# Performance work log

Measured on AMD Instinct MI355X. Metric: run time of the kernel, lower is better.

Reference implementation:

```python
import jax, jax.numpy as jnp
import numpy as np

N = 50000      # nodes
E = 800000     # edges
F = 128        # num_features
H = 128        # hidden_channels
L = 3          # num_layers
P = 32         # num_partitions
EPS = 1e-5     # BatchNorm1d eps


def _batchnorm(h):
    # BatchNorm1d(affine=False, track_running_stats=False): batch stats, biased var
    m = jnp.mean(h, axis=0)
    v = jnp.var(h, axis=0)
    return (h - m) * jax.lax.rsqrt(v + EPS)


def setup_inputs() -> dict:
    key = jax.random.key(0)
    ks = jax.random.split(key, 12)
    x = jax.random.normal(ks[0], (N, F), dtype=jnp.float32)
    edge_index = jax.random.randint(ks[1], (2, E), 0, N)
    edge_weights = jax.random.uniform(ks[2], (E,), dtype=jnp.float32)
    partitions = (jax.random.uniform(ks[3], (N, P)) < (1.0 / P)).astype(jnp.float32)
    node_weights = jax.random.uniform(ks[4], (N,), dtype=jnp.float32)
    edge_curr_node = jax.random.uniform(ks[5], (N,), dtype=jnp.float32)
    conv_w = 0.05 * jax.random.normal(ks[6], (L, F, H), dtype=jnp.float32)
    conv_b = jnp.zeros((L, H), dtype=jnp.float32)
    lin1_w = 0.05 * jax.random.normal(ks[7], (4 * H, H), dtype=jnp.float32)
    lin1_b = jnp.zeros((H,), dtype=jnp.float32)
    lin2_w = 0.05 * jax.random.normal(ks[8], (H, 1), dtype=jnp.float32)
    lin2_b = jnp.zeros((1,), dtype=jnp.float32)
    return {"x": x, "edge_index": edge_index, "edge_weights": edge_weights,
            "partitions": partitions, "node_weights": node_weights,
            "edge_curr_node": edge_curr_node, "conv_w": conv_w, "conv_b": conv_b,
            "lin1_w": lin1_w, "lin1_b": lin1_b, "lin2_w": lin2_w,
            "lin2_b": lin2_b, "curr_node_id": 123}


def reference(x, edge_index, edge_weights, partitions, node_weights,
              edge_curr_node, conv_w, conv_b, lin1_w, lin1_b, lin2_w, lin2_b,
              curr_node_id):
    src, dst = edge_index[0], edge_index[1]
    # GCN normalization with added self-loops (weight 1)
    deg = jax.ops.segment_sum(edge_weights, dst, num_segments=N) + 1.0
    dinv = jax.lax.rsqrt(deg)
    norm = dinv[src] * edge_weights * dinv[dst]          # [E]
    self_norm = (dinv * dinv)[:, None]                   # [N,1]

    h = x
    for l in range(L):
        hw = h @ conv_w[l] + conv_b[l]                   # [N,H]
        agg = jax.ops.segment_sum(hw[src] * norm[:, None], dst, num_segments=N)
        agg = agg + hw * self_norm                       # self-loop term
        h = jax.nn.relu(_batchnorm(agg))

    x_curr = h[curr_node_id]                             # [H]
    # mlp scoring: concat [h | x_curr | edge_col repeated to 2H] -> [N,4H]
    cat = jnp.concatenate([
        h,
        jnp.broadcast_to(x_curr[None, :], (N, H)),
        jnp.broadcast_to(edge_curr_node[:, None], (N, 2 * H)),
    ], axis=1)
    scores = jax.nn.relu(cat @ lin1_w + lin1_b) @ lin2_w + lin2_b  # [N,1]
    # pool == 'sum'
    partition_scores = scores.T @ partitions             # [1,P]
    return (partition_scores, h)
```

## Files before the change

### kernel.cpp

```cpp
#include <hip/hip_runtime.h>

#define N_NODES 50000
#define N_EDGES 800000
#define NP 50048
#define MAXDEG 64
#define PADK 136
#define NCOPY 64
#define WPB 512
#define NBUK 196
#define BCAP 6144
#define EBB 782

typedef __bf16 bf16_8 __attribute__((ext_vector_type(8)));
typedef float  f32_4  __attribute__((ext_vector_type(4)));

__device__ inline float2 bf2f2(unsigned int u) {
    union { unsigned int i; float f; } a, b;
    a.i = u << 16;
    b.i = u & 0xffff0000u;
    return make_float2(a.f, b.f);
}

__global__ void k_init_wprep(float* __restrict__ colpart, float* __restrict__ out_head,
                             const float* __restrict__ conv_w, const float* __restrict__ lin1_w,
                             __bf16* __restrict__ WT, float* __restrict__ svec,
                             int* __restrict__ bcnt) {
    int b = blockIdx.x, t = threadIdx.x;
    if (b < WPB) {
        int mat = b >> 7, n = b & 127;
        if (t < 128) {
            const float* srcm = (mat < 3) ? (conv_w + (size_t)mat * 16384) : lin1_w;
            WT[((size_t)mat * 128 + n) * 128 + t] = (__bf16)srcm[(size_t)t * 128 + n];
        }
    } else if (b == WPB) {
        if (t < 128) {
            float s = 0.f;
            for (int k = 256; k < 512; ++k) s += lin1_w[(size_t)k * 128 + t];
            svec[t] = s;
        }
    } else if (b < WPB + 65) {
        int i = (b - WPB - 1) * 256 + t;
        colpart[i] = 0.f;
    } else {
        if (t < 32) out_head[t] = 0.f;
        for (int i = t; i < NBUK * 16; i += 256) bcnt[i] = 0;
    }
}

__global__ __launch_bounds__(1024) void k_bucket(const int* __restrict__ src,
                                                 const int* __restrict__ dst,
                                                 const float* __restrict__ ew,
                                                 int* __restrict__ bcnt,
                                                 uint2* __restrict__ ebuf) {
    __shared__ uint2 stage[1024];
    __shared__ int cnt[NBUK], cnt2[NBUK], lstart[NBUK], gb[NBUK];
    __shared__ int wtot[4];
    int t = threadIdx.x;
    int e0 = blockIdx.x * 1024;
    int tot = min(1024, N_EDGES - e0);
    if (t < NBUK) { cnt[t] = 0; cnt2[t] = 0; }
    __syncthreads();
    uint2 rec = make_uint2(0u, 0u); int b = -1;
    if (t < tot) {
        int e = e0 + t;
        unsigned s = (unsigned)src[e], d = (unsigned)dst[e];
        rec = make_uint2(s | (d << 16), __float_as_uint(ew[e]));
        b = (int)(d >> 8);
        atomicAdd(&cnt[b], 1);
    }
    __syncthreads();
    int c = (t < NBUK) ? cnt[t] : 0;
    int x = c;
#pragma unroll
    for (int d2 = 1; d2 < 64; d2 <<= 1) {
        int v = __shfl_up(x, d2, 64);
        if ((t & 63) >= d2) x += v;
    }
    if ((t & 63) == 63 && t < 256) wtot[t >> 6] = x;
    if (t < NBUK && c > 0) gb[t] = atomicAdd(&bcnt[t * 16], c);
    __syncthreads();
    if (t < NBUK) {
        int pre = x - c;
        for (int w = 0; w < (t >> 6); ++w) pre += wtot[w];
        lstart[t] = pre;
    }
    __syncthreads();
    if (t < tot) {
        int r = atomicAdd(&cnt2[b], 1);
        stage[lstart[b] + r] = rec;
    }
    __syncthreads();
    if (t < tot) {
        uint2 v = stage[t];
        int bb = (int)(v.x >> 24);
        int idx = gb[bb] + (t - lstart[bb]);
        if (idx < BCAP) ebuf[(size_t)bb * BCAP + idx] = v;
    }
}

__global__ __launch_bounds__(256) void k_build(const int* __restrict__ bcnt,
                                               const uint2* __restrict__ ebuf,
                                               uint2* __restrict__ esn,
                                               int* __restrict__ fillp,
                                               float* __restrict__ dinv) {
    __shared__ int cnt[256];
    __shared__ float wsum[256];
    int t = threadIdx.x, b = blockIdx.x;
    cnt[t] = 0; wsum[t] = 0.f;
    __syncthreads();
    int m = min(bcnt[b * 16], BCAP);
    for (int i = t; i < m; i += 256) {
        uint2 rec = ebuf[(size_t)b * BCAP + i];
        int d = (int)(rec.x >> 16);
        int local = d & 255;
        int pos = atomicAdd(&cnt[local], 1);
        if (pos < MAXDEG)
            esn[(size_t)d * MAXDEG + pos] = make_uint2(rec.x & 0xffffu, rec.y);
        atomicAdd(&wsum[local], __uint_as_float(rec.y));
    }
    __syncthreads();
    int gn = b * 256 + t;
    if (gn < N_NODES) {
        fillp[gn] = cnt[t];
        dinv[gn] = rsqrtf(1.0f + wsum[t]);
    }
}

__global__ __launch_bounds__(256) void k_wnorm(uint2* __restrict__ esn,
                                               const int* __restrict__ fillp,
                                               const float* __restrict__ dinv) {
    int t = threadIdx.x;
    int n = (blockIdx.x * 256 + t) >> 6;
    int lane = t & 63;
    if (n >= N_NODES) return;
    int num = min(fillp[n], MAXDEG);
    if (lane < num) {
        uint2 e = esn[(size_t)n * MAXDEG + lane];
        float w = dinv[(int)e.x] * __uint_as_float(e.y) * dinv[n];
        esn[(size_t)n * MAXDEG + lane] = make_uint2(e.x, __float_as_uint(w));
    }
}

template <int AMODE>
__global__ __launch_bounds__(256) void k_gemm_mfma(const float* __restrict__ A,
                                                   const float* __restrict__ mean,
                                                   const float* __restrict__ rstd,
                                                   const __bf16* __restrict__ WT,
                                                   const float* __restrict__ bias,
                                                   __bf16* __restrict__ C, int nrows) {
    __shared__ __bf16 As[64 * PADK];
    __shared__ __bf16 Ws[128 * PADK];
    int t = threadIdx.x;
    int rowBase = blockIdx.x * 64;
    const uint4* WTg = (const uint4*)WT;
    for (int i = t; i < 2048; i += 256) {
        int n = i >> 4, k8 = i & 15;
        *(uint4*)&Ws[n * PADK + k8 * 8] = WTg[i];
    }
    const float4* A4 = (const float4*)A;
    const float4* M4 = (const float4*)mean;
    const float4* R4 = (const float4*)rstd;
    for (int i = t; i < 1024; i += 256) {
        int r = i >> 4, k8 = i & 15;
        int gr = rowBase + r;
        float4 a0 = make_float4(0.f, 0.f, 0.f, 0.f), a1 = a0;
        if (gr < nrows) {
            a0 = A4[(size_t)gr * 32 + k8 * 2];
            a1 = A4[(size_t)gr * 32 + k8 * 2 + 1];
        }
        if (AMODE == 1) {
            float4 m0 = M4[k8 * 2], m1 = M4[k8 * 2 + 1];
            float4 r0 = R4[k8 * 2], r1 = R4[k8 * 2 + 1];
            a0.x = fmaxf((a0.x - m0.x) * r0.x, 0.f); a0.y = fmaxf((a0.y - m0.y) * r0.y, 0.f);
            a0.z = fmaxf((a0.z - m0.z) * r0.z, 0.f); a0.w = fmaxf((a0.w - m0.w) * r0.w, 0.f);
            a1.x = fmaxf((a1.x - m1.x) * r1.x, 0.f); a1.y = fmaxf((a1.y - m1.y) * r1.y, 0.f);
            a1.z = fmaxf((a1.z - m1.z) * r1.z, 0.f); a1.w = fmaxf((a1.w - m1.w) * r1.w, 0.f);
        }
        bf16_8 o = { (__bf16)a0.x, (__bf16)a0.y, (__bf16)a0.z, (__bf16)a0.w,
                     (__bf16)a1.x, (__bf16)a1.y, (__bf16)a1.z, (__bf16)a1.w };
        *(bf16_8*)&As[r * PADK + k8 * 8] = o;
    }
    __syncthreads();
    int wave = t >> 6, lane = t & 63, quad = lane >> 4, m = lane & 15;
    int ar = wave * 16 + m;
    f32_4 acc[8];
#pragma unroll
    for (int i = 0; i < 8; ++i) acc[i] = (f32_4){0.f, 0.f, 0.f, 0.f};
#pragma unroll
    for (int kk = 0; kk < 4; ++kk) {
        bf16_8 a = *(const bf16_8*)&As[ar * PADK + kk * 32 + quad * 8];
#pragma unroll
        for (int n0 = 0; n0 < 8; ++n0) {
            bf16_8 b = *(const bf16_8*)&Ws[(n0 * 16 + m) * PADK + kk * 32 + quad * 8];
            acc[n0] = __builtin_amdgcn_mfma_f32_16x16x32_bf16(a, b, acc[n0], 0, 0, 0);
        }
    }
    __syncthreads();
#pragma unroll
    for (int n0 = 0; n0 < 8; ++n0) {
        int col = n0 * 16 + m;
        float bi = bias[col];
#pragma unroll
        for (int r = 0; r < 4; ++r) {
            int rr = wave * 16 + quad * 4 + r;
            As[rr * PADK + col] = (__bf16)(acc[n0][r] + bi);
        }
    }
    __syncthreads();
    uint4* Cg = (uint4*)C;
    for (int i = t; i < 1024; i += 256) {
        int r = i >> 4, k8 = i & 15;
        int gr = rowBase + r;
        if (gr < nrows) Cg[(size_t)gr * 16 + k8] = *(const uint4*)&As[r * PADK + k8 * 8];
    }
}

__global__ __launch_bounds__(256) void k_agg(const __bf16* __restrict__ hwb,
                                             const uint2* __restrict__ esn,
                                             const int* __restrict__ fillp,
                                             const float* __restrict__ dinv,
                                             float* __restrict__ agg,
                                             float* __restrict__ colpart) {
    __shared__ float red1[4 * 128], red2[4 * 128];
    int t = threadIdx.x;
    int n = (blockIdx.x * 256 + t) >> 6;
    int lane = t & 63, wave = t >> 6;
    float2 acc = make_float2(0.f, 0.f);
    const unsigned int* hw32 = (const unsigned int*)hwb;
    if (n < N_NODES) {
        float dvn = dinv[n];
        float2 sv = bf2f2(hw32[(size_t)n * 64 + lane]);
        acc.x = sv.x * dvn * dvn; acc.y = sv.y * dvn * dvn;
        int num = min(fillp[n], MAXDEG);
        int s_l = 0; float w_l = 0.f;
        if (lane < num) {
            uint2 e = esn[(size_t)n * MAXDEG + lane];
            s_l = (int)e.x;
            w_l = __uint_as_float(e.y);
        }
        int i = 0;
        for (; i + 8 <= num; i += 8) {
            int ss[8]; float ww[8]; unsigned uu[8];
#pragma unroll
            for (int j = 0; j < 8; ++j) { ss[j] = __shfl(s_l, i + j); ww[j] = __shfl(w_l, i + j); }
#pragma unroll
            for (int j = 0; j < 8; ++j) uu[j] = hw32[(size_t)ss[j] * 64 + lane];
#pragma unroll
            for (int j = 0; j < 8; ++j) {
                float2 f = bf2f2(uu[j]);
                acc.x += f.x * ww[j]; acc.y += f.y * ww[j];
            }
        }
        for (; i < num; ++i) {
            int s = __shfl(s_l, i);
            float w = __shfl(w_l, i);
            float2 f = bf2f2(hw32[(size_t)s * 64 + lane]);
            acc.x += f.x * w; acc.y += f.y * w;
        }
        ((float2*)agg)[(size_t)n * 64 + lane] = acc;
    }
    *(float2*)&red1[wave * 128 + 2 * lane] = acc;
    *(float2*)&red2[wave * 128 + 2 * lane] = make_float2(acc.x * acc.x, acc.y * acc.y);
    __syncthreads();
    if (t < 128) {
        float s = red1[t] + red1[128 + t] + red1[256 + t] + red1[384 + t];
        float q = red2[t] + red2[128 + t] + red2[256 + t] + red2[384 + t];
        int c = blockIdx.x & (NCOPY - 1);
        unsafeAtomicAdd(&colpart[c * 128 + t], s);
        unsafeAtomicAdd(&colpart[NCOPY * 128 + c * 128 + t], q);
    }
}

__global__ void k_bnfinal(float* colpart, float* mean, float* rstd) {
    int j = threadIdx.x;
    float s = 0.f, q = 0.f;
    for (int c = 0; c < NCOPY; ++c) {
        s += colpart[c * 128 + j];
        q += colpart[NCOPY * 128 + c * 128 + j];
        colpart[c * 128 + j] = 0.f;
        colpart[NCOPY * 128 + c * 128 + j] = 0.f;
    }
    float m = s * (1.0f / N_NODES);
    float v = q * (1.0f / N_NODES) - m * m;
    mean[j] = m;
    rstd[j] = rsqrtf(v + 1e-5f);
}

__global__ void k_prep(const float* __restrict__ agg, const float* __restrict__ mean,
                       const float* __restrict__ rstd, const int* __restrict__ cid,
                       const float* __restrict__ lin1w, const float* __restrict__ lin1b,
                       float* c0) {
    __shared__ float xc[128];
    int t = threadIdx.x;
    int cn = cid[0];
    float a = agg[(size_t)cn * 128 + t];
    xc[t] = fmaxf((a - mean[t]) * rstd[t], 0.f);
    __syncthreads();
    float acc = lin1b[t];
    for (int k = 0; k < 128; ++k)
        acc += xc[k] * lin1w[(size_t)(128 + k) * 128 + t];
    c0[t] = acc;
}

__global__ __launch_bounds__(256) void k_score_mfma(const float* __restrict__ agg,
                                                    const float* __restrict__ mean,
                                                    const float* __restrict__ rstd,
                                                    const __bf16* __restrict__ WT,
                                                    const float* __restrict__ c0,
                                                    const float* __restrict__ svec,
                                                    const float* __restrict__ ecn,
                                                    const float* __restrict__ lin2w,
                                                    const float* __restrict__ lin2b,
                                                    float* __restrict__ scores,
                                                    float* __restrict__ hout,
                                                    int nrows) {
    __shared__ __bf16 As[64 * PADK];
    __shared__ __bf16 Ws[128 * PADK];
    __shared__ float c0s[128], svs[128], l2s[128];
    int t = threadIdx.x;
    int rowBase = blockIdx.x * 64;
    const uint4* WTg = (const uint4*)WT;
    for (int i = t; i < 2048; i += 256) {
        int n = i >> 4, k8 = i & 15;
        *(uint4*)&Ws[n * PADK + k8 * 8] = WTg[i];
    }
    const float4* A4 = (const float4*)agg;
    const float4* M4 = (const float4*)mean;
    const float4* R4 = (const float4*)rstd;
    float4* H4 = (float4*)hout;
    for (int i = t; i < 1024; i += 256) {
        int r = i >> 4, k8 = i & 15;
        int gr = rowBase + r;
        float4 a0 = make_float4(0.f, 0.f, 0.f, 0.f), a1 = a0;
        if (gr < nrows) {
            a0 = A4[(size_t)gr * 32 + k8 * 2];
            a1 = A4[(size_t)gr * 32 + k8 * 2 + 1];
        }
        float4 m0 = M4[k8 * 2], m1 = M4[k8 * 2 + 1];
        float4 r0 = R4[k8 * 2], r1 = R4[k8 * 2 + 1];
        float4 f0, f1;
        f0.x = fmaxf((a0.x - m0.x) * r0.x, 0.f); f0.y = fmaxf((a0.y - m0.y) * r0.y, 0.f);
        f0.z = fmaxf((a0.z - m0.z) * r0.z, 0.f); f0.w = fmaxf((a0.w - m0.w) * r0.w, 0.f);
        f1.x = fmaxf((a1.x - m1.x) * r1.x, 0.f); f1.y = fmaxf((a1.y - m1.y) * r1.y, 0.f);
        f1.z = fmaxf((a1.z - m1.z) * r1.z, 0.f); f1.w = fmaxf((a1.w - m1.w) * r1.w, 0.f);
        if (gr < nrows) {
            H4[(size_t)gr * 32 + k8 * 2] = f0;
            H4[(size_t)gr * 32 + k8 * 2 + 1] = f1;
        }
        bf16_8 o = { (__bf16)f0.x, (__bf16)f0.y, (__bf16)f0.z, (__bf16)f0.w,
                     (__bf16)f1.x, (__bf16)f1.y, (__bf16)f1.z, (__bf16)f1.w };
        *(bf16_8*)&As[r * PADK + k8 * 8] = o;
    }
    if (t < 128) { c0s[t] = c0[t]; svs[t] = svec[t]; l2s[t] = lin2w[t]; }
    __syncthreads();
    int wave = t >> 6, lane = t & 63, quad = lane >> 4, m = lane & 15;
    int ar = wave * 16 + m;
    f32_4 acc[8];
#pragma unroll
    for (int i = 0; i < 8; ++i) acc[i] = (f32_4){0.f, 0.f, 0.f, 0.f};
#pragma unroll
    for (int kk = 0; kk < 4; ++kk) {
        bf16_8 a = *(const bf16_8*)&As[ar * PADK + kk * 32 + quad * 8];
#pragma unroll
        for (int n0 = 0; n0 < 8; ++n0) {
            bf16_8 b = *(const bf16_8*)&Ws[(n0 * 16 + m) * PADK + kk * 32 + quad * 8];
            acc[n0] = __builtin_amdgcn_mfma_f32_16x16x32_bf16(a, b, acc[n0], 0, 0, 0);
        }
    }
    float l2b = lin2b[0];
#pragma unroll
    for (int r = 0; r < 4; ++r) {
        int row = rowBase + wave * 16 + quad * 4 + r;
        float e = (row < nrows) ? ecn[row] : 0.f;
        float partial = 0.f;
#pragma unroll
        for (int n0 = 0; n0 < 8; ++n0) {
            int col = n0 * 16 + m;
            float v = acc[n0][r] + c0s[col] + e * svs[col];
            partial += fmaxf(v, 0.f) * l2s[col];
        }
        partial += __shfl_xor(partial, 8, 16);
        partial += __shfl_xor(partial, 4, 16);
        partial += __shfl_xor(partial, 2, 16);
        partial += __shfl_xor(partial, 1, 16);
        if (m == 0 && row < nrows) scores[row] = partial + l2b;
    }
}

__global__ void k_partition(const float* __restrict__ scores, const float* __restrict__ part,
                            float* out) {
    __shared__ float red[256];
    int t = threadIdx.x;
    int p = t & 31, rg = t >> 5;
    float acc = 0.f;
    for (int r = blockIdx.x * 8 + rg; r < N_NODES; r += gridDim.x * 8)
        acc += scores[r] * part[(size_t)r * 32 + p];
    red[t] = acc;
    __syncthreads();
    if (t < 32) {
        float s = 0.f;
        for (int i = 0; i < 8; ++i) s += red[i * 32 + t];
        unsafeAtomicAdd(&out[t], s);
    }
}

extern "C" void kernel_launch(void* const* d_in, const int* in_sizes, int n_in,
                              void* d_out, int out_size, void* d_ws, size_t ws_size,
                              hipStream_t stream) {
    const float* x        = (const float*)d_in[0];
    const int*   eidx     = (const int*)d_in[1];
    const float* ew       = (const float*)d_in[2];
    const float* parts    = (const float*)d_in[3];
    const float* ecn      = (const float*)d_in[5];
    const float* conv_w   = (const float*)d_in[6];
    const float* conv_b   = (const float*)d_in[7];
    const float* lin1_w   = (const float*)d_in[8];
    const float* lin1_b   = (const float*)d_in[9];
    const float* lin2_w   = (const float*)d_in[10];
    const float* lin2_b   = (const float*)d_in[11];
    const int*   cid      = (const int*)d_in[12];

    const int* src = eidx;
    const int* dst = eidx + N_EDGES;

    char* p = (char*)d_ws;
    auto alloc = [&](size_t bytes) { char* r = p; p += (bytes + 255) & ~size_t(255); return r; };
    int*    fillp   = (int*)alloc((size_t)NP * 4);
    uint2*  esn     = (uint2*)alloc((size_t)N_NODES * MAXDEG * 8);
    float*  dinv    = (float*)alloc(NP * 4);
    float*  scores  = (float*)alloc(NP * 4);
    float*  colpart = (float*)alloc(2 * NCOPY * 128 * 4);
    float*  mean    = (float*)alloc(128 * 4);
    float*  rstd    = (float*)alloc(128 * 4);
    float*  c0      = (float*)alloc(128 * 4);
    float*  svec    = (float*)alloc(128 * 4);
    __bf16* WT      = (__bf16*)alloc(4 * 128 * 128 * 2);
    __bf16* hwb     = (__bf16*)alloc((size_t)N_NODES * 128 * 2);
    float*  agg     = (float*)alloc((size_t)N_NODES * 128 * 4);
    int*    bcnt    = (int*)alloc((size_t)NBUK * 16 * 4);
    uint2*  ebuf    = (uint2*)alloc((size_t)NBUK * BCAP * 8);

    float* out_head = (float*)d_out;
    float* hbuf     = (float*)d_out + 32;

    const int GB = (N_NODES + 63) / 64;
    const int AB = (N_NODES * 64 + 255) / 256;

    k_init_wprep<<<WPB + 66, 256, 0, stream>>>(colpart, out_head, conv_w, lin1_w, WT, svec, bcnt);
    k_bucket<<<EBB, 1024, 0, stream>>>(src, dst, ew, bcnt, ebuf);
    k_build<<<NBUK, 256, 0, stream>>>(bcnt, ebuf, esn, fillp, dinv);
    k_wnorm<<<AB, 256, 0, stream>>>(esn, fillp, dinv);

    for (int l = 0; l < 3; ++l) {
        if (l == 0)
            k_gemm_mfma<0><<<GB, 256, 0, stream>>>(x, mean, rstd, WT, conv_b, hwb, N_NODES);
        else
            k_gemm_mfma<1><<<GB, 256, 0, stream>>>(agg, mean, rstd, WT + (size_t)l * 16384,
                                                   conv_b + (size_t)l * 128, hwb, N_NODES);
        k_agg<<<AB, 256, 0, stream>>>(hwb, esn, fillp, dinv, agg, colpart);
        k_bnfinal<<<1, 128, 0, stream>>>(colpart, mean, rstd);
    }

    k_prep<<<1, 128, 0, stream>>>(agg, mean, rstd, cid, lin1_w, lin1_b, c0);
    k_score_mfma<<<GB, 256, 0, stream>>>(agg, mean, rstd, WT + (size_t)3 * 16384, c0, svec,
                                         ecn, lin2_w, lin2_b, scores, hbuf, N_NODES);
    k_partition<<<256, 256, 0, stream>>>(scores, parts, out_head);
}
```

Measured before the change: 347.8 us.

## Gather 16-byte neighbor rows in aggregation and fuse edge-normalization into first GEMM

The aggregation kernel now gives each lane 8 bf16 features loaded as a uint4, so each wave processes 4 neighbors at once in 16-lane groups. The partial sums are then combined with cross-lane xor shuffles, which cuts the number of gather instructions and shuffles per edge. Separately, the edge-weight normalization kernel becomes extra blocks appended to the layer-0 GEMM launch, which removes one launch and lets that work overlap with the GEMM. The cost is more registers per thread, the shuffle reduction overhead, and shared-memory declarations in the normalization blocks that they do not use.

```diff
diff --git a/kernel.cpp b/kernel.cpp
--- a/kernel.cpp
+++ b/kernel.cpp
@@ -126,31 +126,32 @@
     }
 }
 
-__global__ __launch_bounds__(256) void k_wnorm(uint2* __restrict__ esn,
-                                               const int* __restrict__ fillp,
-                                               const float* __restrict__ dinv) {
-    int t = threadIdx.x;
-    int n = (blockIdx.x * 256 + t) >> 6;
-    int lane = t & 63;
-    if (n >= N_NODES) return;
-    int num = min(fillp[n], MAXDEG);
-    if (lane < num) {
-        uint2 e = esn[(size_t)n * MAXDEG + lane];
-        float w = dinv[(int)e.x] * __uint_as_float(e.y) * dinv[n];
-        esn[(size_t)n * MAXDEG + lane] = make_uint2(e.x, __float_as_uint(w));
-    }
-}
-
 template <int AMODE>
 __global__ __launch_bounds__(256) void k_gemm_mfma(const float* __restrict__ A,
                                                    const float* __restrict__ mean,
                                                    const float* __restrict__ rstd,
                                                    const __bf16* __restrict__ WT,
                                                    const float* __restrict__ bias,
-                                                   __bf16* __restrict__ C, int nrows) {
+                                                   __bf16* __restrict__ C, int nrows,
+                                                   uint2* __restrict__ esn,
+                                                   const int* __restrict__ fillp,
+                                                   const float* __restrict__ dinv,
+                                                   int gemmBlocks) {
     __shared__ __bf16 As[64 * PADK];
     __shared__ __bf16 Ws[128 * PADK];
     int t = threadIdx.x;
+    if (AMODE == 0 && blockIdx.x >= gemmBlocks) {
+        int n = ((blockIdx.x - gemmBlocks) * 256 + t) >> 6;
+        int lane = t & 63;
+        if (n >= N_NODES) return;
+        int num = min(fillp[n], MAXDEG);
+        if (lane < num) {
+            uint2 e = esn[(size_t)n * MAXDEG + lane];
+            float w = dinv[(int)e.x] * __uint_as_float(e.y) * dinv[n];
+            esn[(size_t)n * MAXDEG + lane] = make_uint2(e.x, __float_as_uint(w));
+        }
+        return;
+    }
     int rowBase = blockIdx.x * 64;
     const uint4* WTg = (const uint4*)WT;
     for (int i = t; i < 2048; i += 256) {
@@ -225,42 +226,80 @@
     int t = threadIdx.x;
     int n = (blockIdx.x * 256 + t) >> 6;
     int lane = t & 63, wave = t >> 6;
-    float2 acc = make_float2(0.f, 0.f);
-    const unsigned int* hw32 = (const unsigned int*)hwb;
+    int rs = lane >> 4, c16 = lane & 15;
+    float acc[8];
+#pragma unroll
+    for (int k = 0; k < 8; ++k) acc[k] = 0.f;
+    const uint4* hwq = (const uint4*)hwb;
     if (n < N_NODES) {
+        int num = min(fillp[n], MAXDEG);
         float dvn = dinv[n];
-        float2 sv = bf2f2(hw32[(size_t)n * 64 + lane]);
-        acc.x = sv.x * dvn * dvn; acc.y = sv.y * dvn * dvn;
-        int num = min(fillp[n], MAXDEG);
+        uint4 sv = hwq[(size_t)n * 16 + c16];
         int s_l = 0; float w_l = 0.f;
         if (lane < num) {
             uint2 e = esn[(size_t)n * MAXDEG + lane];
             s_l = (int)e.x;
             w_l = __uint_as_float(e.y);
         }
-        int i = 0;
-        for (; i + 8 <= num; i += 8) {
-            int ss[8]; float ww[8]; unsigned uu[8];
-#pragma unroll
-            for (int j = 0; j < 8; ++j) { ss[j] = __shfl(s_l, i + j); ww[j] = __shfl(w_l, i + j); }
-#pragma unroll
-            for (int j = 0; j < 8; ++j) uu[j] = hw32[(size_t)ss[j] * 64 + lane];
-#pragma unroll
-            for (int j = 0; j < 8; ++j) {
-                float2 f = bf2f2(uu[j]);
-                acc.x += f.x * ww[j]; acc.y += f.y * ww[j];
+        int groups = (num + 3) >> 2;
+        int g = 0;
+        for (; g + 4 <= groups; g += 4) {
+            uint4 u[4]; float w[4];
+#pragma unroll
+            for (int j = 0; j < 4; ++j) {
+                int idx = (g + j) * 4 + rs;
+                int s = __shfl(s_l, idx, 64);
+                w[j] = __shfl(w_l, idx, 64);
+                u[j] = hwq[(size_t)s * 16 + c16];
             }
-        }
-        for (; i < num; ++i) {
-            int s = __shfl(s_l, i);
-            float w = __shfl(w_l, i);
-            float2 f = bf2f2(hw32[(size_t)s * 64 + lane]);
-            acc.x += f.x * w; acc.y += f.y * w;
-        }
-        ((float2*)agg)[(size_t)n * 64 + lane] = acc;
-    }
-    *(float2*)&red1[wave * 128 + 2 * lane] = acc;
-    *(float2*)&red2[wave * 128 + 2 * lane] = make_float2(acc.x * acc.x, acc.y * acc.y);
+#pragma unroll
+            for (int j = 0; j < 4; ++j) {
+                float2 f0 = bf2f2(u[j].x), f1 = bf2f2(u[j].y);
+                float2 f2 = bf2f2(u[j].z), f3 = bf2f2(u[j].w);
+                acc[0] += f0.x * w[j]; acc[1] += f0.y * w[j];
+                acc[2] += f1.x * w[j]; acc[3] += f1.y * w[j];
+                acc[4] += f2.x * w[j]; acc[5] += f2.y * w[j];
+                acc[6] += f3.x * w[j]; acc[7] += f3.y * w[j];
+            }
+        }
+        for (; g < groups; ++g) {
+            int idx = g * 4 + rs;
+            int s = __shfl(s_l, idx, 64);
+            float w = __shfl(w_l, idx, 64);
+            uint4 u = hwq[(size_t)s * 16 + c16];
+            float2 f0 = bf2f2(u.x), f1 = bf2f2(u.y), f2 = bf2f2(u.z), f3 = bf2f2(u.w);
+            acc[0] += f0.x * w; acc[1] += f0.y * w;
+            acc[2] += f1.x * w; acc[3] += f1.y * w;
+            acc[4] += f2.x * w; acc[5] += f2.y * w;
+            acc[6] += f3.x * w; acc[7] += f3.y * w;
+        }
+#pragma unroll
+        for (int k = 0; k < 8; ++k) {
+            acc[k] += __shfl_xor(acc[k], 16, 64);
+            acc[k] += __shfl_xor(acc[k], 32, 64);
+        }
+        float d2 = dvn * dvn;
+        float2 s0 = bf2f2(sv.x), s1 = bf2f2(sv.y), s2 = bf2f2(sv.z), s3 = bf2f2(sv.w);
+        acc[0] += s0.x * d2; acc[1] += s0.y * d2;
+        acc[2] += s1.x * d2; acc[3] += s1.y * d2;
+        acc[4] += s2.x * d2; acc[5] += s2.y * d2;
+        acc[6] += s3.x * d2; acc[7] += s3.y * d2;
+        if (rs < 2) {
+            float4 o = make_float4(acc[rs * 4 + 0], acc[rs * 4 + 1],
+                                   acc[rs * 4 + 2], acc[rs * 4 + 3]);
+            ((float4*)agg)[(size_t)n * 32 + c16 * 2 + rs] = o;
+        }
+    }
+    if (rs == 0) {
+        *(float4*)&red1[wave * 128 + c16 * 8 + 0] =
+            make_float4(acc[0], acc[1], acc[2], acc[3]);
+        *(float4*)&red1[wave * 128 + c16 * 8 + 4] =
+            make_float4(acc[4], acc[5], acc[6], acc[7]);
+        *(float4*)&red2[wave * 128 + c16 * 8 + 0] =
+            make_float4(acc[0] * acc[0], acc[1] * acc[1], acc[2] * acc[2], acc[3] * acc[3]);
+        *(float4*)&red2[wave * 128 + c16 * 8 + 4] =
+            make_float4(acc[4] * acc[4], acc[5] * acc[5], acc[6] * acc[6], acc[7] * acc[7]);
+    }
     __syncthreads();
     if (t < 128) {
         float s = red1[t] + red1[128 + t] + red1[256 + t] + red1[384 + t];
@@ -449,14 +488,15 @@
     k_init_wprep<<<WPB + 66, 256, 0, stream>>>(colpart, out_head, conv_w, lin1_w, WT, svec, bcnt);
     k_bucket<<<EBB, 1024, 0, stream>>>(src, dst, ew, bcnt, ebuf);
     k_build<<<NBUK, 256, 0, stream>>>(bcnt, ebuf, esn, fillp, dinv);
-    k_wnorm<<<AB, 256, 0, stream>>>(esn, fillp, dinv);
 
     for (int l = 0; l < 3; ++l) {
         if (l == 0)
-            k_gemm_mfma<0><<<GB, 256, 0, stream>>>(x, mean, rstd, WT, conv_b, hwb, N_NODES);
+            k_gemm_mfma<0><<<GB + AB, 256, 0, stream>>>(x, mean, rstd, WT, conv_b, hwb, N_NODES,
+                                                        esn, fillp, dinv, GB);
         else
             k_gemm_mfma<1><<<GB, 256, 0, stream>>>(agg, mean, rstd, WT + (size_t)l * 16384,
-                                                   conv_b + (size_t)l * 128, hwb, N_NODES);
+                                                   conv_b + (size_t)l * 128, hwb, N_NODES,
+                                                   nullptr, nullptr, nullptr, GB);
         k_agg<<<AB, 256, 0, stream>>>(hwb, esn, fillp, dinv, agg, colpart);
         k_bnfinal<<<1, 128, 0, stream>>>(colpart, mean, rstd);
     }
```

New measurement: 344.3 us. Within noise of the previous version (-1.0%).

## Pack edges into CSR layout, fuse weight-normalization into first GEMM, split aggregation by feature chunk

Applied to the files above, without the earlier changes.

Replaces the padded per-node 64-slot edge array with a compact CSR-style packed array built by a prefix scan in k_build. The separate edge-weight normalization kernel is folded into extra blocks of the first GEMM launch, which removes one launch and lets that work overlap the GEMM. k_agg is restructured so each block handles one 32-column feature chunk, with blocks mapped across XCDs by chunk for better L2 locality of the gathered rows. Each wave processes four edges at a time in 16-lane groups and combines them with cross-lane shuffles. This adds launch blocks and shuffle reductions in exchange for less padded memory traffic and better cache reuse.

```diff
diff --git a/kernel.cpp b/kernel.cpp
--- a/kernel.cpp
+++ b/kernel.cpp
@@ -10,6 +10,7 @@
 #define NBUK 196
 #define BCAP 6144
 #define EBB 782
+#define AGB 50000
 
 typedef __bf16 bf16_8 __attribute__((ext_vector_type(8)));
 typedef float  f32_4  __attribute__((ext_vector_type(4)));
@@ -100,44 +101,50 @@
 
 __global__ __launch_bounds__(256) void k_build(const int* __restrict__ bcnt,
                                                const uint2* __restrict__ ebuf,
-                                               uint2* __restrict__ esn,
+                                               uint2* __restrict__ packed,
+                                               int* __restrict__ rowofs,
                                                int* __restrict__ fillp,
                                                float* __restrict__ dinv) {
     __shared__ int cnt[256];
     __shared__ float wsum[256];
+    __shared__ int pos[256];
+    __shared__ int wtot[4];
     int t = threadIdx.x, b = blockIdx.x;
     cnt[t] = 0; wsum[t] = 0.f;
     __syncthreads();
     int m = min(bcnt[b * 16], BCAP);
     for (int i = t; i < m; i += 256) {
         uint2 rec = ebuf[(size_t)b * BCAP + i];
-        int d = (int)(rec.x >> 16);
-        int local = d & 255;
-        int pos = atomicAdd(&cnt[local], 1);
-        if (pos < MAXDEG)
-            esn[(size_t)d * MAXDEG + pos] = make_uint2(rec.x & 0xffffu, rec.y);
+        int local = (int)(rec.x >> 16) & 255;
+        atomicAdd(&cnt[local], 1);
         atomicAdd(&wsum[local], __uint_as_float(rec.y));
     }
     __syncthreads();
+    int c = cnt[t];
+    int x = c;
+#pragma unroll
+    for (int d2 = 1; d2 < 64; d2 <<= 1) {
+        int v = __shfl_up(x, d2, 64);
+        if ((t & 63) >= d2) x += v;
+    }
+    if ((t & 63) == 63) wtot[t >> 6] = x;
+    __syncthreads();
+    int pre = x - c;
+    for (int w = 0; w < (t >> 6); ++w) pre += wtot[w];
+    int rstart = b * BCAP + pre;
+    pos[t] = rstart;
+    __syncthreads();
+    for (int i = t; i < m; i += 256) {
+        uint2 rec = ebuf[(size_t)b * BCAP + i];
+        int local = (int)(rec.x >> 16) & 255;
+        int p = atomicAdd(&pos[local], 1);
+        packed[p] = make_uint2(rec.x & 0xffffu, rec.y);
+    }
     int gn = b * 256 + t;
     if (gn < N_NODES) {
-        fillp[gn] = cnt[t];
+        fillp[gn] = c;
+        rowofs[gn] = rstart;
         dinv[gn] = rsqrtf(1.0f + wsum[t]);
-    }
-}
-
-__global__ __launch_bounds__(256) void k_wnorm(uint2* __restrict__ esn,
-                                               const int* __restrict__ fillp,
-                                               const float* __restrict__ dinv) {
-    int t = threadIdx.x;
-    int n = (blockIdx.x * 256 + t) >> 6;
-    int lane = t & 63;
-    if (n >= N_NODES) return;
-    int num = min(fillp[n], MAXDEG);
-    if (lane < num) {
-        uint2 e = esn[(size_t)n * MAXDEG + lane];
-        float w = dinv[(int)e.x] * __uint_as_float(e.y) * dinv[n];
-        esn[(size_t)n * MAXDEG + lane] = make_uint2(e.x, __float_as_uint(w));
     }
 }
 
@@ -147,10 +154,28 @@
                                                    const float* __restrict__ rstd,
                                                    const __bf16* __restrict__ WT,
                                                    const float* __restrict__ bias,
-                                                   __bf16* __restrict__ C, int nrows) {
+                                                   __bf16* __restrict__ C, int nrows,
+                                                   uint2* __restrict__ packed,
+                                                   const int* __restrict__ rowofs,
+                                                   const int* __restrict__ fillp,
+                                                   const float* __restrict__ dinv,
+                                                   int gemmBlocks) {
     __shared__ __bf16 As[64 * PADK];
     __shared__ __bf16 Ws[128 * PADK];
     int t = threadIdx.x;
+    if (AMODE == 0 && blockIdx.x >= gemmBlocks) {
+        int n = ((blockIdx.x - gemmBlocks) * 256 + t) >> 6;
+        int lane = t & 63;
+        if (n >= N_NODES) return;
+        int num = min(fillp[n], MAXDEG);
+        if (lane < num) {
+            int ro = rowofs[n];
+            uint2 e = packed[ro + lane];
+            float w = dinv[(int)e.x] * __uint_as_float(e.y) * dinv[n];
+            packed[ro + lane] = make_uint2(e.x, __float_as_uint(w));
+        }
+        return;
+    }
     int rowBase = blockIdx.x * 64;
     const uint4* WTg = (const uint4*)WT;
     for (int i = t; i < 2048; i += 256) {
@@ -216,58 +241,79 @@
 }
 
 __global__ __launch_bounds__(256) void k_agg(const __bf16* __restrict__ hwb,
-                                             const uint2* __restrict__ esn,
+                                             const uint2* __restrict__ packed,
+                                             const int* __restrict__ rowofs,
                                              const int* __restrict__ fillp,
                                              const float* __restrict__ dinv,
                                              float* __restrict__ agg,
                                              float* __restrict__ colpart) {
-    __shared__ float red1[4 * 128], red2[4 * 128];
+    __shared__ float red1[4 * 32], red2[4 * 32];
     int t = threadIdx.x;
-    int n = (blockIdx.x * 256 + t) >> 6;
+    int bi = blockIdx.x;
+    int xcd = bi & 7;
+    int chunk = xcd >> 1;
+    int nb = (bi >> 3) * 2 + (xcd & 1);
     int lane = t & 63, wave = t >> 6;
+    int e4 = lane >> 4, f16 = lane & 15;
+    int n = nb * 4 + wave;
     float2 acc = make_float2(0.f, 0.f);
     const unsigned int* hw32 = (const unsigned int*)hwb;
-    if (n < N_NODES) {
+    {
+        int num = min(fillp[n], MAXDEG);
+        int ro = rowofs[n];
         float dvn = dinv[n];
-        float2 sv = bf2f2(hw32[(size_t)n * 64 + lane]);
-        acc.x = sv.x * dvn * dvn; acc.y = sv.y * dvn * dvn;
-        int num = min(fillp[n], MAXDEG);
+        unsigned sv = hw32[(size_t)n * 64 + chunk * 16 + f16];
         int s_l = 0; float w_l = 0.f;
         if (lane < num) {
-            uint2 e = esn[(size_t)n * MAXDEG + lane];
+            uint2 e = packed[ro + lane];
             s_l = (int)e.x;
             w_l = __uint_as_float(e.y);
         }
-        int i = 0;
-        for (; i + 8 <= num; i += 8) {
-            int ss[8]; float ww[8]; unsigned uu[8];
-#pragma unroll
-            for (int j = 0; j < 8; ++j) { ss[j] = __shfl(s_l, i + j); ww[j] = __shfl(w_l, i + j); }
-#pragma unroll
-            for (int j = 0; j < 8; ++j) uu[j] = hw32[(size_t)ss[j] * 64 + lane];
-#pragma unroll
-            for (int j = 0; j < 8; ++j) {
-                float2 f = bf2f2(uu[j]);
-                acc.x += f.x * ww[j]; acc.y += f.y * ww[j];
+        int groups = (num + 3) >> 2;
+        int g = 0;
+        for (; g + 4 <= groups; g += 4) {
+            unsigned u[4]; float w[4];
+#pragma unroll
+            for (int j = 0; j < 4; ++j) {
+                int idx = (g + j) * 4 + e4;
+                int s = __shfl(s_l, idx, 64);
+                w[j] = __shfl(w_l, idx, 64);
+                u[j] = hw32[(size_t)s * 64 + chunk * 16 + f16];
             }
-        }
-        for (; i < num; ++i) {
-            int s = __shfl(s_l, i);
-            float w = __shfl(w_l, i);
-            float2 f = bf2f2(hw32[(size_t)s * 64 + lane]);
+#pragma unroll
+            for (int j = 0; j < 4; ++j) {
+                float2 f = bf2f2(u[j]);
+                acc.x += f.x * w[j]; acc.y += f.y * w[j];
+            }
+        }
+        for (; g < groups; ++g) {
+            int idx = g * 4 + e4;
+            int s = __shfl(s_l, idx, 64);
+            float w = __shfl(w_l, idx, 64);
+            float2 f = bf2f2(hw32[(size_t)s * 64 + chunk * 16 + f16]);
             acc.x += f.x * w; acc.y += f.y * w;
         }
-        ((float2*)agg)[(size_t)n * 64 + lane] = acc;
-    }
-    *(float2*)&red1[wave * 128 + 2 * lane] = acc;
-    *(float2*)&red2[wave * 128 + 2 * lane] = make_float2(acc.x * acc.x, acc.y * acc.y);
-    __syncthreads();
-    if (t < 128) {
-        float s = red1[t] + red1[128 + t] + red1[256 + t] + red1[384 + t];
-        float q = red2[t] + red2[128 + t] + red2[256 + t] + red2[384 + t];
+        acc.x += __shfl_xor(acc.x, 16, 64); acc.y += __shfl_xor(acc.y, 16, 64);
+        acc.x += __shfl_xor(acc.x, 32, 64); acc.y += __shfl_xor(acc.y, 32, 64);
+        float d2 = dvn * dvn;
+        float2 s0 = bf2f2(sv);
+        acc.x += s0.x * d2; acc.y += s0.y * d2;
+        if (e4 == 0)
+            ((float2*)agg)[(size_t)n * 64 + chunk * 16 + f16] = acc;
+    }
+    if (e4 == 0) {
+        red1[wave * 32 + f16 * 2]     = acc.x;
+        red1[wave * 32 + f16 * 2 + 1] = acc.y;
+        red2[wave * 32 + f16 * 2]     = acc.x * acc.x;
+        red2[wave * 32 + f16 * 2 + 1] = acc.y * acc.y;
+    }
+    __syncthreads();
+    if (t < 32) {
+        float s = red1[t] + red1[32 + t] + red1[64 + t] + red1[96 + t];
+        float q = red2[t] + red2[32 + t] + red2[64 + t] + red2[96 + t];
         int c = blockIdx.x & (NCOPY - 1);
-        unsafeAtomicAdd(&colpart[c * 128 + t], s);
-        unsafeAtomicAdd(&colpart[NCOPY * 128 + c * 128 + t], q);
+        unsafeAtomicAdd(&colpart[c * 128 + chunk * 32 + t], s);
+        unsafeAtomicAdd(&colpart[NCOPY * 128 + c * 128 + chunk * 32 + t], q);
     }
 }
 
@@ -426,7 +472,8 @@
     char* p = (char*)d_ws;
     auto alloc = [&](size_t bytes) { char* r = p; p += (bytes + 255) & ~size_t(255); return r; };
     int*    fillp   = (int*)alloc((size_t)NP * 4);
-    uint2*  esn     = (uint2*)alloc((size_t)N_NODES * MAXDEG * 8);
+    int*    rowofs  = (int*)alloc((size_t)NP * 4);
+    uint2*  packed  = (uint2*)alloc((size_t)NBUK * BCAP * 8);
     float*  dinv    = (float*)alloc(NP * 4);
     float*  scores  = (float*)alloc(NP * 4);
     float*  colpart = (float*)alloc(2 * NCOPY * 128 * 4);
@@ -448,16 +495,17 @@
 
     k_init_wprep<<<WPB + 66, 256, 0, stream>>>(colpart, out_head, conv_w, lin1_w, WT, svec, bcnt);
     k_bucket<<<EBB, 1024, 0, stream>>>(src, dst, ew, bcnt, ebuf);
-    k_build<<<NBUK, 256, 0, stream>>>(bcnt, ebuf, esn, fillp, dinv);
-    k_wnorm<<<AB, 256, 0, stream>>>(esn, fillp, dinv);
+    k_build<<<NBUK, 256, 0, stream>>>(bcnt, ebuf, packed, rowofs, fillp, dinv);
 
     for (int l = 0; l < 3; ++l) {
         if (l == 0)
-            k_gemm_mfma<0><<<GB, 256, 0, stream>>>(x, mean, rstd, WT, conv_b, hwb, N_NODES);
+            k_gemm_mfma<0><<<GB + AB, 256, 0, stream>>>(x, mean, rstd, WT, conv_b, hwb, N_NODES,
+                                                        packed, rowofs, fillp, dinv, GB);
         else
             k_gemm_mfma<1><<<GB, 256, 0, stream>>>(agg, mean, rstd, WT + (size_t)l * 16384,
-                                                   conv_b + (size_t)l * 128, hwb, N_NODES);
-        k_agg<<<AB, 256, 0, stream>>>(hwb, esn, fillp, dinv, agg, colpart);
+                                                   conv_b + (size_t)l * 128, hwb, N_NODES,
+                                                   nullptr, nullptr, nullptr, nullptr, GB);
+        k_agg<<<AGB, 256, 0, stream>>>(hwb, packed, rowofs, fillp, dinv, agg, colpart);
         k_bnfinal<<<1, 128, 0, stream>>>(colpart, mean, rstd);
     }
 
```

Result: slower. 452.5 us (+30.1%).
